# Performance work log

Hardware: AMD Instinct MI355X
Metric: run time of the kernel (lower is better)

The kernel has to match this reference:

```python
import jax, jax.numpy as jnp
import numpy as np

DIM = 256; H = 64; W = 64; NH = 8; NL = 1; NP = 8; HD = DIM // NH
B = 4


def _bilinear(img, grid):
    """torch.grid_sample(mode='bilinear', padding='zeros', align_corners=False).
    img: [C, Hl, Wl]; grid: [N, P, 2] normalized xy in [-1, 1]. Returns [C, N, P]."""
    Hl, Wl = img.shape[1], img.shape[2]
    x = (grid[..., 0] + 1.0) * (Wl * 0.5) - 0.5
    y = (grid[..., 1] + 1.0) * (Hl * 0.5) - 0.5
    x0 = jnp.floor(x); y0 = jnp.floor(y)
    wx = x - x0; wy = y - y0

    def gather(xi, yi):
        valid = (xi >= 0) & (xi < Wl) & (yi >= 0) & (yi < Hl)
        xc = jnp.clip(xi, 0, Wl - 1).astype(jnp.int32)
        yc = jnp.clip(yi, 0, Hl - 1).astype(jnp.int32)
        return img[:, yc, xc] * valid.astype(img.dtype)[None]  # [C, N, P]

    v00 = gather(x0, y0); v01 = gather(x0 + 1, y0)
    v10 = gather(x0, y0 + 1); v11 = gather(x0 + 1, y0 + 1)
    top = v00 * (1.0 - wx) + v01 * wx
    bot = v10 * (1.0 - wx) + v11 * wx
    return top * (1.0 - wy) + bot * wy


def _msda(value, loc, att):
    """multi_scale_deformable_attn_pytorch.
    value: [b, nv, NH, HD]; loc: [b, nq, NH, NL, NP, 2] in [0,1]; att: [b, nq, NH, NL, NP]."""
    b, nv, _, _ = value.shape
    nq = loc.shape[1]
    grids = 2.0 * loc - 1.0
    bn = b * NH
    level_shapes = [(H, W)] * NL  # all levels share the single [H, W] grid here
    sampled_levels = []
    offset = 0
    for l, (Hl, Wl) in enumerate(level_shapes):
        vl = value[:, offset:offset + Hl * Wl]                     # [b, HW, NH, HD]
        offset += Hl * Wl
        vl = vl.transpose(0, 2, 3, 1).reshape(bn, HD, Hl, Wl)      # [b*NH, HD, Hl, Wl]
        gl = grids[:, :, :, l].transpose(0, 2, 1, 3, 4).reshape(bn, nq, NP, 2)
        sampled_levels.append(jax.vmap(_bilinear)(vl, gl))         # [b*NH, HD, nq, NP]
    sampled = jnp.stack(sampled_levels, axis=3)                    # [b*NH, HD, nq, NL, NP]
    w = att.transpose(0, 2, 1, 3, 4).reshape(bn, 1, nq, NL, NP)
    out = jnp.sum(sampled * w, axis=(3, 4))                        # [b*NH, HD, nq]
    return out.reshape(b, NH, HD, nq).transpose(0, 3, 1, 2).reshape(b, nq, NH * HD)


def _forward(query, value, W_loc, b_loc, W_att, b_att, W_val, b_val, W_out, b_out):
    b = query.shape[0]
    nq = H * W
    q = query.transpose(0, 2, 3, 1).reshape(b, nq, DIM)
    v = value.transpose(0, 2, 3, 1).reshape(b, nq, DIM)
    loc = (q @ W_loc.T + b_loc).reshape(b, nq, NH, NL, NP, 2)
    att = jax.nn.softmax((q @ W_att.T + b_att).reshape(b, nq, NH, NL * NP), axis=-1)
    att = att.reshape(b, nq, NH, NL, NP)
    v = (v @ W_val.T + b_val).reshape(b, nq, NH, HD)
    out = _msda(v, loc, att)                                       # [b, nq, DIM]
    return out @ W_out.T + b_out


def setup_inputs() -> dict:
    key = jax.random.key(0)
    ks = jax.random.split(key, 12)
    s = 0.02
    return {
        "query": jax.random.normal(ks[0], (B, DIM, H, W), jnp.float32),
        "value": jax.random.normal(ks[1], (B, DIM, H, W), jnp.float32),
        "W_loc": jax.random.normal(ks[2], (NH * NL * NP * 2, DIM), jnp.float32) * s,
        "b_loc": jax.random.normal(ks[3], (NH * NL * NP * 2,), jnp.float32) * s,
        "W_att": jax.random.normal(ks[4], (NH * NL * NP, DIM), jnp.float32) * s,
        "b_att": jax.random.normal(ks[5], (NH * NL * NP,), jnp.float32) * s,
        "W_val": jax.random.normal(ks[6], (DIM, DIM), jnp.float32) * s,
        "b_val": jax.random.normal(ks[7], (DIM,), jnp.float32) * s,
        "W_out": jax.random.normal(ks[8], (DIM, DIM), jnp.float32) * s,
        "b_out": jax.random.normal(ks[9], (DIM,), jnp.float32) * s,
    }


def reference(query, value, W_loc, b_loc, W_att, b_att, W_val, b_val, W_out, b_out):
    return _forward(query, value, W_loc, b_loc, W_att, b_att, W_val, b_val, W_out, b_out)
```

## Files before the change

### kernel.cpp

```cpp
#include <hip/hip_runtime.h>
#include <hip/hip_bf16.h>
#include <math.h>

#define NQ   4096
#define DIMC 256
#define NHC  8
#define NPC  8
#define HDC  32
#define HC   64
#define WC   64
#define BC   4

typedef __bf16 bf16x8 __attribute__((ext_vector_type(8)));
typedef __attribute__((ext_vector_type(4))) float f4;
typedef __attribute__((ext_vector_type(2))) float v2f;
typedef __attribute__((ext_vector_type(8))) short s8v;

__device__ __forceinline__ ushort f2bf(float f) {
  __hip_bfloat16 h = __float2bfloat16(f);
  union { __hip_bfloat16 h; ushort u; } c; c.h = h; return c.u;
}
__device__ __forceinline__ float bflo(unsigned u) {
  union { unsigned i; float f; } c; c.i = u << 16; return c.f;
}
__device__ __forceinline__ float bfhi(unsigned u) {
  union { unsigned i; float f; } c; c.i = u & 0xffff0000u; return c.f;
}

__global__ __launch_bounds__(256) void k_locatt(
    const float* __restrict__ query,
    const float* __restrict__ W_loc, const float* __restrict__ b_loc,
    const float* __restrict__ W_att, const float* __restrict__ b_att,
    float* __restrict__ loc, float* __restrict__ att) {
  __shared__ float Xs[16][136];
  __shared__ float Ws[16][72];
  const int b  = blockIdx.z;
  const int n0 = blockIdx.x * 128;
  const int o0 = blockIdx.y * 64;
  const int tid = threadIdx.x;
  const int xk = tid >> 4, xn = (tid & 15) * 8;
  const int wo = tid >> 2, wk = (tid & 3) * 4;
  const int tn = (tid & 15) * 8;
  const int to = (tid >> 4) * 4;
  const float* Xb = query + (size_t)b * DIMC * NQ;
  const int oo = o0 + wo;
  const float* Wrow = (oo < 128) ? (W_loc + (size_t)oo * DIMC)
                                 : (W_att + (size_t)(oo - 128) * DIMC);

  v2f acc[8][2];
#pragma unroll
  for (int i = 0; i < 8; ++i) { acc[i][0] = (v2f)0.f; acc[i][1] = (v2f)0.f; }

  for (int k0 = 0; k0 < DIMC; k0 += 16) {
    float4 xv0 = *(const float4*)(Xb + (size_t)(k0 + xk) * NQ + n0 + xn);
    float4 xv1 = *(const float4*)(Xb + (size_t)(k0 + xk) * NQ + n0 + xn + 4);
    float4 wv  = *(const float4*)(Wrow + k0 + wk);
    __syncthreads();
    *(float4*)(&Xs[xk][xn])     = xv0;
    *(float4*)(&Xs[xk][xn + 4]) = xv1;
    Ws[wk + 0][wo] = wv.x; Ws[wk + 1][wo] = wv.y;
    Ws[wk + 2][wo] = wv.z; Ws[wk + 3][wo] = wv.w;
    __syncthreads();
#pragma unroll
    for (int k = 0; k < 16; ++k) {
      float4 xa = *(const float4*)(&Xs[k][tn]);
      float4 xb = *(const float4*)(&Xs[k][tn + 4]);
      v2f w01 = *(const v2f*)(&Ws[k][to]);
      v2f w23 = *(const v2f*)(&Ws[k][to + 2]);
      float xr[8] = {xa.x, xa.y, xa.z, xa.w, xb.x, xb.y, xb.z, xb.w};
#pragma unroll
      for (int i = 0; i < 8; ++i) {
        v2f xi = {xr[i], xr[i]};
        acc[i][0] = xi * w01 + acc[i][0];
        acc[i][1] = xi * w23 + acc[i][1];
      }
    }
  }
  const int obase = o0 + to;
  if (obase < 128) {
    float4 bias = *(const float4*)(b_loc + obase);
#pragma unroll
    for (int i = 0; i < 8; ++i) {
      const int n = n0 + tn + i;
      float4 r = {acc[i][0].x + bias.x, acc[i][0].y + bias.y,
                  acc[i][1].x + bias.z, acc[i][1].y + bias.w};
      *(float4*)(loc + ((size_t)b * NQ + n) * 128 + obase) = r;
    }
  } else {
    float4 bias = *(const float4*)(b_att + obase - 128);
#pragma unroll
    for (int i = 0; i < 8; ++i) {
      const int n = n0 + tn + i;
      float4 r = {acc[i][0].x + bias.x, acc[i][0].y + bias.y,
                  acc[i][1].x + bias.z, acc[i][1].y + bias.w};
      *(float4*)(att + ((size_t)b * NQ + n) * 64 + obase - 128) = r;
    }
  }
}

#define LSTR 40
__global__ __launch_bounds__(256) void k_vproj(
    const float* __restrict__ value, const float* __restrict__ W_val,
    const float* __restrict__ b_val, ushort* __restrict__ vproj) {
  __shared__ __align__(16) ushort As[128 * LSTR];
  __shared__ __align__(16) ushort Ws[64 * LSTR];
  const int b  = blockIdx.z;
  const int n0 = blockIdx.x * 128;
  const int o0 = blockIdx.y * 64;
  const int tid = threadIdx.x;
  const int lane = tid & 63, wid = tid >> 6;
  const int wn0 = (wid & 1) * 64, wo0 = (wid >> 1) * 32;
  const int an = tid & 31;
  const int ak = (tid >> 5) * 4;
  const int wo = tid >> 2, wk = (tid & 3) * 8;
  const float* Xb = value + (size_t)b * DIMC * NQ;
  const int am = lane & 15, kq = (lane >> 4) * 8;

  f4 acc[4][2];
#pragma unroll
  for (int mi = 0; mi < 4; ++mi) { acc[mi][0] = (f4)0.f; acc[mi][1] = (f4)0.f; }

  for (int k0 = 0; k0 < DIMC; k0 += 32) {
    float av[4][4];
#pragma unroll
    for (int kk = 0; kk < 4; ++kk)
#pragma unroll
      for (int nn = 0; nn < 4; ++nn)
        av[kk][nn] = Xb[(size_t)(k0 + ak + kk) * NQ + n0 + an + nn * 32];
    float4 w0 = *(const float4*)(W_val + (size_t)(o0 + wo) * DIMC + k0 + wk);
    float4 w1 = *(const float4*)(W_val + (size_t)(o0 + wo) * DIMC + k0 + wk + 4);
    __syncthreads();
#pragma unroll
    for (int nn = 0; nn < 4; ++nn) {
      ushort4 pk;
      pk.x = f2bf(av[0][nn]); pk.y = f2bf(av[1][nn]);
      pk.z = f2bf(av[2][nn]); pk.w = f2bf(av[3][nn]);
      *(ushort4*)(&As[(an + nn * 32) * LSTR + ak]) = pk;
    }
    {
      ushort4 pa, pb;
      pa.x = f2bf(w0.x); pa.y = f2bf(w0.y); pa.z = f2bf(w0.z); pa.w = f2bf(w0.w);
      pb.x = f2bf(w1.x); pb.y = f2bf(w1.y); pb.z = f2bf(w1.z); pb.w = f2bf(w1.w);
      *(ushort4*)(&Ws[wo * LSTR + wk])     = pa;
      *(ushort4*)(&Ws[wo * LSTR + wk + 4]) = pb;
    }
    __syncthreads();
    bf16x8 afr[4], bfr[2];
#pragma unroll
    for (int mi = 0; mi < 4; ++mi)
      afr[mi] = *(const bf16x8*)(&As[(wn0 + mi * 16 + am) * LSTR + kq]);
#pragma unroll
    for (int oj = 0; oj < 2; ++oj)
      bfr[oj] = *(const bf16x8*)(&Ws[(wo0 + oj * 16 + am) * LSTR + kq]);
#pragma unroll
    for (int mi = 0; mi < 4; ++mi)
#pragma unroll
      for (int oj = 0; oj < 2; ++oj)
        acc[mi][oj] = __builtin_amdgcn_mfma_f32_16x16x32_bf16(
            afr[mi], bfr[oj], acc[mi][oj], 0, 0, 0);
  }
#pragma unroll
  for (int oj = 0; oj < 2; ++oj) {
    const int o = o0 + wo0 + oj * 16 + (lane & 15);
    const int h = o >> 5, d = o & 31;
    const float bias = b_val[o];
    ushort* dst = vproj + ((size_t)(b * NHC + h) * NQ) * HDC + d;
#pragma unroll
    for (int mi = 0; mi < 4; ++mi) {
      const int nb = n0 + wn0 + mi * 16 + (lane >> 4) * 4;
#pragma unroll
      for (int r = 0; r < 4; ++r)
        dst[(size_t)(nb + r) * HDC] = f2bf(acc[mi][oj][r] + bias);
    }
  }
}

__global__ __launch_bounds__(256) void k_sample(
    const float* __restrict__ loc, const float* __restrict__ attL,
    const ushort* __restrict__ vproj, ushort* __restrict__ msda) {
  __shared__ float4 Lc[32][9];
  __shared__ int4   Lo[32][9];
  const int b = blockIdx.z, h = blockIdx.y;
  const int tid = threadIdx.x;
  const int n0 = blockIdx.x * 32;
  {
    const int q = tid >> 3, p = tid & 7;
    const int n = n0 + q;
    const float lg = attL[((size_t)b * NQ + n) * 64 + h * 8 + p];
    float m = lg;
#pragma unroll
    for (int off = 1; off < 8; off <<= 1) m = fmaxf(m, __shfl_xor(m, off, 64));
    const float e = __expf(lg - m);
    float s = e;
#pragma unroll
    for (int off = 1; off < 8; off <<= 1) s += __shfl_xor(s, off, 64);
    const float w = e / s;
    const float2 xy = *(const float2*)(loc + ((size_t)b * NQ + n) * 128 + h * 16 + p * 2);
    const float x = xy.x * 64.0f - 0.5f;
    const float y = xy.y * 64.0f - 0.5f;
    const float x0f = floorf(x), y0f = floorf(y);
    const float wx = x - x0f, wy = y - y0f;
    const int x0 = (int)x0f, y0 = (int)y0f;
    const int x1 = x0 + 1, y1 = y0 + 1;
    const float fx0 = (x0 >= 0 && x0 < WC) ? 1.f : 0.f;
    const float fx1 = (x1 >= 0 && x1 < WC) ? 1.f : 0.f;
    const float fy0 = (y0 >= 0 && y0 < HC) ? 1.f : 0.f;
    const float fy1 = (y1 >= 0 && y1 < HC) ? 1.f : 0.f;
    const int cx0 = min(max(x0, 0), WC - 1), cx1 = min(max(x1, 0), WC - 1);
    const int cy0 = min(max(y0, 0), HC - 1), cy1 = min(max(y1, 0), HC - 1);
    float4 cf;
    cf.x = w * (1.f - wx) * (1.f - wy) * fx0 * fy0;
    cf.y = w * wx * (1.f - wy) * fx1 * fy0;
    cf.z = w * (1.f - wx) * wy * fx0 * fy1;
    cf.w = w * wx * wy * fx1 * fy1;
    int4 of;
    of.x = (cy0 * WC + cx0) * HDC; of.y = (cy0 * WC + cx1) * HDC;
    of.z = (cy1 * WC + cx0) * HDC; of.w = (cy1 * WC + cx1) * HDC;
    Lc[q][p] = cf; Lo[q][p] = of;
  }
  __syncthreads();
  const int q = tid >> 3, d4 = (tid & 7) * 4;
  const int n = n0 + q;
  const ushort* vb = vproj + (size_t)((b * NHC + h) * NQ) * HDC + d4;
  float a0 = 0.f, a1 = 0.f, a2 = 0.f, a3 = 0.f;
#pragma unroll
  for (int p = 0; p < 8; ++p) {
    const int4 of = Lo[q][p];
    const float4 cf = Lc[q][p];
    uint2 u00 = *(const uint2*)(vb + of.x);
    uint2 u01 = *(const uint2*)(vb + of.y);
    uint2 u10 = *(const uint2*)(vb + of.z);
    uint2 u11 = *(const uint2*)(vb + of.w);
    a0 += cf.x * bflo(u00.x) + cf.y * bflo(u01.x) + cf.z * bflo(u10.x) + cf.w * bflo(u11.x);
    a1 += cf.x * bfhi(u00.x) + cf.y * bfhi(u01.x) + cf.z * bfhi(u10.x) + cf.w * bfhi(u11.x);
    a2 += cf.x * bflo(u00.y) + cf.y * bflo(u01.y) + cf.z * bflo(u10.y) + cf.w * bflo(u11.y);
    a3 += cf.x * bfhi(u00.y) + cf.y * bfhi(u01.y) + cf.z * bfhi(u10.y) + cf.w * bfhi(u11.y);
  }
  ushort4 r;
  r.x = f2bf(a0); r.y = f2bf(a1); r.z = f2bf(a2); r.w = f2bf(a3);
  *(ushort4*)(msda + ((size_t)b * NQ + n) * DIMC + h * HDC + d4) = r;
}

__global__ __launch_bounds__(256) void k_out(
    const ushort* __restrict__ msda, const float* __restrict__ W_out,
    const float* __restrict__ b_out, float* __restrict__ out) {
  __shared__ __align__(16) ushort As[128 * LSTR];
  __shared__ __align__(16) ushort Ws[64 * LSTR];
  const int b  = blockIdx.z;
  const int n0 = blockIdx.x * 128;
  const int o0 = blockIdx.y * 64;
  const int tid = threadIdx.x;
  const int lane = tid & 63, wid = tid >> 6;
  const int wn0 = (wid & 1) * 64, wo0 = (wid >> 1) * 32;
  const int ar = tid >> 1, akh = (tid & 1) * 16;
  const int wo = tid >> 2, wk = (tid & 3) * 8;
  const int am = lane & 15, kq = (lane >> 4) * 8;
  const ushort* Ab = msda + (size_t)b * NQ * DIMC;

  f4 acc[4][2];
#pragma unroll
  for (int mi = 0; mi < 4; ++mi) { acc[mi][0] = (f4)0.f; acc[mi][1] = (f4)0.f; }

  for (int k0 = 0; k0 < DIMC; k0 += 32) {
    s8v a0 = *(const s8v*)(Ab + (size_t)(n0 + ar) * DIMC + k0 + akh);
    s8v a1 = *(const s8v*)(Ab + (size_t)(n0 + ar) * DIMC + k0 + akh + 8);
    float4 w0 = *(const float4*)(W_out + (size_t)(o0 + wo) * DIMC + k0 + wk);
    float4 w1 = *(const float4*)(W_out + (size_t)(o0 + wo) * DIMC + k0 + wk + 4);
    __syncthreads();
    *(s8v*)(&As[ar * LSTR + akh])     = a0;
    *(s8v*)(&As[ar * LSTR + akh + 8]) = a1;
    {
      ushort4 pa, pb;
      pa.x = f2bf(w0.x); pa.y = f2bf(w0.y); pa.z = f2bf(w0.z); pa.w = f2bf(w0.w);
      pb.x = f2bf(w1.x); pb.y = f2bf(w1.y); pb.z = f2bf(w1.z); pb.w = f2bf(w1.w);
      *(ushort4*)(&Ws[wo * LSTR + wk])     = pa;
      *(ushort4*)(&Ws[wo * LSTR + wk + 4]) = pb;
    }
    __syncthreads();
    bf16x8 afr[4], bfr[2];
#pragma unroll
    for (int mi = 0; mi < 4; ++mi)
      afr[mi] = *(const bf16x8*)(&As[(wn0 + mi * 16 + am) * LSTR + kq]);
#pragma unroll
    for (int oj = 0; oj < 2; ++oj)
      bfr[oj] = *(const bf16x8*)(&Ws[(wo0 + oj * 16 + am) * LSTR + kq]);
#pragma unroll
    for (int mi = 0; mi < 4; ++mi)
#pragma unroll
      for (int oj = 0; oj < 2; ++oj)
        acc[mi][oj] = __builtin_amdgcn_mfma_f32_16x16x32_bf16(
            afr[mi], bfr[oj], acc[mi][oj], 0, 0, 0);
  }
#pragma unroll
  for (int oj = 0; oj < 2; ++oj) {
    const int o = o0 + wo0 + oj * 16 + (lane & 15);
    const float bias = b_out[o];
#pragma unroll
    for (int mi = 0; mi < 4; ++mi) {
      const int nb = n0 + wn0 + mi * 16 + (lane >> 4) * 4;
#pragma unroll
      for (int r = 0; r < 4; ++r)
        out[((size_t)b * NQ + nb + r) * DIMC + o] = acc[mi][oj][r] + bias;
    }
  }
}

extern "C" void kernel_launch(void* const* d_in, const int* in_sizes, int n_in,
                              void* d_out, int out_size, void* d_ws, size_t ws_size,
                              hipStream_t stream) {
  const float* query = (const float*)d_in[0];
  const float* value = (const float*)d_in[1];
  const float* W_loc = (const float*)d_in[2];
  const float* b_loc = (const float*)d_in[3];
  const float* W_att = (const float*)d_in[4];
  const float* b_att = (const float*)d_in[5];
  const float* W_val = (const float*)d_in[6];
  const float* b_val = (const float*)d_in[7];
  const float* W_out = (const float*)d_in[8];
  const float* b_out = (const float*)d_in[9];
  float* out = (float*)d_out;

  float* ws = (float*)d_ws;
  float* loc   = ws;
  float* att   = loc + (size_t)BC * NQ * 128;
  ushort* vproj = (ushort*)(att + (size_t)BC * NQ * 64);
  ushort* msda  = vproj + (size_t)BC * NHC * NQ * HDC;

  dim3 blk(256);
  k_locatt<<<dim3(NQ / 128, 3, BC), blk, 0, stream>>>(query, W_loc, b_loc, W_att, b_att, loc, att);
  k_vproj <<<dim3(NQ / 128, 4, BC), blk, 0, stream>>>(value, W_val, b_val, vproj);
  k_sample<<<dim3(NQ / 32, NHC, BC), blk, 0, stream>>>(loc, att, vproj, msda);
  k_out   <<<dim3(NQ / 128, 4, BC), blk, 0, stream>>>(msda, W_out, b_out, out);
}
```

Baseline: 156.7 us.

## Use split-bf16 MFMA for loc/att GEMM, prefetch tiles, shrink GEMM tiles, widen sampling

The FP32 FMA loc/att projection becomes an MFMA GEMM that splits each operand into high and low bf16 parts and uses three MFMAs per tile to keep near-fp32 accuracy on sampling locations. All three GEMMs move to 64x64 tiles with register prefetch of the next k-slice, overlapping global loads with compute and doubling the block count. The sampling kernel handles 64 queries per block, and each thread gathers 8 bf16 channels with 16-byte loads. The split-precision path costs three MFMAs and extra LDS traffic, and smaller tiles reduce per-block reuse.

```diff
diff --git a/kernel.cpp b/kernel.cpp
--- a/kernel.cpp
+++ b/kernel.cpp
@@ -10,15 +10,18 @@
 #define HC   64
 #define WC   64
 #define BC   4
+#define LSTR 40
 
 typedef __bf16 bf16x8 __attribute__((ext_vector_type(8)));
 typedef __attribute__((ext_vector_type(4))) float f4;
-typedef __attribute__((ext_vector_type(2))) float v2f;
 typedef __attribute__((ext_vector_type(8))) short s8v;
 
 __device__ __forceinline__ ushort f2bf(float f) {
   __hip_bfloat16 h = __float2bfloat16(f);
   union { __hip_bfloat16 h; ushort u; } c; c.h = h; return c.u;
+}
+__device__ __forceinline__ float bfu2f(ushort u) {
+  union { unsigned i; float f; } c; c.i = ((unsigned)u) << 16; return c.f;
 }
 __device__ __forceinline__ float bflo(unsigned u) {
   union { unsigned i; float f; } c; c.i = u << 16; return c.f;
@@ -32,141 +35,167 @@
     const float* __restrict__ W_loc, const float* __restrict__ b_loc,
     const float* __restrict__ W_att, const float* __restrict__ b_att,
     float* __restrict__ loc, float* __restrict__ att) {
-  __shared__ float Xs[16][136];
-  __shared__ float Ws[16][72];
-  const int b  = blockIdx.z;
-  const int n0 = blockIdx.x * 128;
-  const int o0 = blockIdx.y * 64;
-  const int tid = threadIdx.x;
-  const int xk = tid >> 4, xn = (tid & 15) * 8;
-  const int wo = tid >> 2, wk = (tid & 3) * 4;
-  const int tn = (tid & 15) * 8;
-  const int to = (tid >> 4) * 4;
-  const float* Xb = query + (size_t)b * DIMC * NQ;
+  __shared__ __align__(16) ushort Ah[64 * LSTR], Al[64 * LSTR];
+  __shared__ __align__(16) ushort Wh[64 * LSTR], Wl[64 * LSTR];
+  const int b = blockIdx.z, n0 = blockIdx.x * 64, o0 = blockIdx.y * 64;
+  const int tid = threadIdx.x, lane = tid & 63, wid = tid >> 6;
+  const int wn0 = (wid & 1) * 32, wo0 = (wid >> 1) * 32;
+  const int am = lane & 15, kq = (lane >> 4) * 8;
+  const int an = tid & 63, ak = (tid >> 6) * 8;
+  const int wo = tid >> 2, wk = (tid & 3) * 8;
+  const float* Xb = query + (size_t)b * DIMC * NQ + n0 + an;
   const int oo = o0 + wo;
   const float* Wrow = (oo < 128) ? (W_loc + (size_t)oo * DIMC)
                                  : (W_att + (size_t)(oo - 128) * DIMC);
 
-  v2f acc[8][2];
-#pragma unroll
-  for (int i = 0; i < 8; ++i) { acc[i][0] = (v2f)0.f; acc[i][1] = (v2f)0.f; }
-
-  for (int k0 = 0; k0 < DIMC; k0 += 16) {
-    float4 xv0 = *(const float4*)(Xb + (size_t)(k0 + xk) * NQ + n0 + xn);
-    float4 xv1 = *(const float4*)(Xb + (size_t)(k0 + xk) * NQ + n0 + xn + 4);
-    float4 wv  = *(const float4*)(Wrow + k0 + wk);
-    __syncthreads();
-    *(float4*)(&Xs[xk][xn])     = xv0;
-    *(float4*)(&Xs[xk][xn + 4]) = xv1;
-    Ws[wk + 0][wo] = wv.x; Ws[wk + 1][wo] = wv.y;
-    Ws[wk + 2][wo] = wv.z; Ws[wk + 3][wo] = wv.w;
-    __syncthreads();
-#pragma unroll
-    for (int k = 0; k < 16; ++k) {
-      float4 xa = *(const float4*)(&Xs[k][tn]);
-      float4 xb = *(const float4*)(&Xs[k][tn + 4]);
-      v2f w01 = *(const v2f*)(&Ws[k][to]);
-      v2f w23 = *(const v2f*)(&Ws[k][to + 2]);
-      float xr[8] = {xa.x, xa.y, xa.z, xa.w, xb.x, xb.y, xb.z, xb.w};
-#pragma unroll
-      for (int i = 0; i < 8; ++i) {
-        v2f xi = {xr[i], xr[i]};
-        acc[i][0] = xi * w01 + acc[i][0];
-        acc[i][1] = xi * w23 + acc[i][1];
+  f4 acc[2][2];
+#pragma unroll
+  for (int mi = 0; mi < 2; ++mi) { acc[mi][0] = (f4)0.f; acc[mi][1] = (f4)0.f; }
+
+  float ax[8];
+  float4 wx0, wx1;
+#pragma unroll
+  for (int j = 0; j < 8; ++j) ax[j] = Xb[(size_t)(ak + j) * NQ];
+  wx0 = *(const float4*)(Wrow + wk);
+  wx1 = *(const float4*)(Wrow + wk + 4);
+
+  for (int t = 0; t < 8; ++t) {
+    __syncthreads();
+    {
+      union { ushort u[8]; s8v s; } ph, pl;
+#pragma unroll
+      for (int j = 0; j < 8; ++j) {
+        ushort h = f2bf(ax[j]);
+        ph.u[j] = h;
+        pl.u[j] = f2bf(ax[j] - bfu2f(h));
       }
-    }
-  }
-  const int obase = o0 + to;
-  if (obase < 128) {
-    float4 bias = *(const float4*)(b_loc + obase);
-#pragma unroll
-    for (int i = 0; i < 8; ++i) {
-      const int n = n0 + tn + i;
-      float4 r = {acc[i][0].x + bias.x, acc[i][0].y + bias.y,
-                  acc[i][1].x + bias.z, acc[i][1].y + bias.w};
-      *(float4*)(loc + ((size_t)b * NQ + n) * 128 + obase) = r;
-    }
-  } else {
-    float4 bias = *(const float4*)(b_att + obase - 128);
-#pragma unroll
-    for (int i = 0; i < 8; ++i) {
-      const int n = n0 + tn + i;
-      float4 r = {acc[i][0].x + bias.x, acc[i][0].y + bias.y,
-                  acc[i][1].x + bias.z, acc[i][1].y + bias.w};
-      *(float4*)(att + ((size_t)b * NQ + n) * 64 + obase - 128) = r;
-    }
-  }
-}
-
-#define LSTR 40
+      *(s8v*)(&Ah[an * LSTR + ak]) = ph.s;
+      *(s8v*)(&Al[an * LSTR + ak]) = pl.s;
+      float wt[8] = {wx0.x, wx0.y, wx0.z, wx0.w, wx1.x, wx1.y, wx1.z, wx1.w};
+      union { ushort u[8]; s8v s; } qh, ql;
+#pragma unroll
+      for (int j = 0; j < 8; ++j) {
+        ushort h = f2bf(wt[j]);
+        qh.u[j] = h;
+        ql.u[j] = f2bf(wt[j] - bfu2f(h));
+      }
+      *(s8v*)(&Wh[wo * LSTR + wk]) = qh.s;
+      *(s8v*)(&Wl[wo * LSTR + wk]) = ql.s;
+    }
+    if (t < 7) {
+      const int k0 = (t + 1) * 32;
+#pragma unroll
+      for (int j = 0; j < 8; ++j) ax[j] = Xb[(size_t)(k0 + ak + j) * NQ];
+      wx0 = *(const float4*)(Wrow + k0 + wk);
+      wx1 = *(const float4*)(Wrow + k0 + wk + 4);
+    }
+    __syncthreads();
+    bf16x8 ah[2], al[2], bh[2], bl[2];
+#pragma unroll
+    for (int mi = 0; mi < 2; ++mi) {
+      ah[mi] = *(const bf16x8*)(&Ah[(wn0 + mi * 16 + am) * LSTR + kq]);
+      al[mi] = *(const bf16x8*)(&Al[(wn0 + mi * 16 + am) * LSTR + kq]);
+    }
+#pragma unroll
+    for (int oj = 0; oj < 2; ++oj) {
+      bh[oj] = *(const bf16x8*)(&Wh[(wo0 + oj * 16 + am) * LSTR + kq]);
+      bl[oj] = *(const bf16x8*)(&Wl[(wo0 + oj * 16 + am) * LSTR + kq]);
+    }
+#pragma unroll
+    for (int mi = 0; mi < 2; ++mi)
+#pragma unroll
+      for (int oj = 0; oj < 2; ++oj) {
+        acc[mi][oj] = __builtin_amdgcn_mfma_f32_16x16x32_bf16(ah[mi], bh[oj], acc[mi][oj], 0, 0, 0);
+        acc[mi][oj] = __builtin_amdgcn_mfma_f32_16x16x32_bf16(al[mi], bh[oj], acc[mi][oj], 0, 0, 0);
+        acc[mi][oj] = __builtin_amdgcn_mfma_f32_16x16x32_bf16(ah[mi], bl[oj], acc[mi][oj], 0, 0, 0);
+      }
+  }
+  const bool isAtt = (o0 >= 128);
+  float* dstBase = isAtt ? att : loc;
+  const float* bias = isAtt ? b_att : b_loc;
+  const int ostride = isAtt ? 64 : 128;
+  const int ob = isAtt ? o0 - 128 : o0;
+#pragma unroll
+  for (int oj = 0; oj < 2; ++oj) {
+    const int o = ob + wo0 + oj * 16 + am;
+    const float bv = bias[o];
+#pragma unroll
+    for (int mi = 0; mi < 2; ++mi) {
+      const int nb = n0 + wn0 + mi * 16 + (lane >> 4) * 4;
+#pragma unroll
+      for (int r = 0; r < 4; ++r)
+        dstBase[((size_t)b * NQ + nb + r) * ostride + o] = acc[mi][oj][r] + bv;
+    }
+  }
+}
+
 __global__ __launch_bounds__(256) void k_vproj(
     const float* __restrict__ value, const float* __restrict__ W_val,
     const float* __restrict__ b_val, ushort* __restrict__ vproj) {
-  __shared__ __align__(16) ushort As[128 * LSTR];
+  __shared__ __align__(16) ushort As[64 * LSTR];
   __shared__ __align__(16) ushort Ws[64 * LSTR];
-  const int b  = blockIdx.z;
-  const int n0 = blockIdx.x * 128;
-  const int o0 = blockIdx.y * 64;
-  const int tid = threadIdx.x;
-  const int lane = tid & 63, wid = tid >> 6;
-  const int wn0 = (wid & 1) * 64, wo0 = (wid >> 1) * 32;
-  const int an = tid & 31;
-  const int ak = (tid >> 5) * 4;
+  const int b = blockIdx.z, n0 = blockIdx.x * 64, o0 = blockIdx.y * 64;
+  const int tid = threadIdx.x, lane = tid & 63, wid = tid >> 6;
+  const int wn0 = (wid & 1) * 32, wo0 = (wid >> 1) * 32;
+  const int am = lane & 15, kq = (lane >> 4) * 8;
+  const int an = tid & 63, ak = (tid >> 6) * 8;
   const int wo = tid >> 2, wk = (tid & 3) * 8;
-  const float* Xb = value + (size_t)b * DIMC * NQ;
-  const int am = lane & 15, kq = (lane >> 4) * 8;
-
-  f4 acc[4][2];
-#pragma unroll
-  for (int mi = 0; mi < 4; ++mi) { acc[mi][0] = (f4)0.f; acc[mi][1] = (f4)0.f; }
-
-  for (int k0 = 0; k0 < DIMC; k0 += 32) {
-    float av[4][4];
-#pragma unroll
-    for (int kk = 0; kk < 4; ++kk)
-#pragma unroll
-      for (int nn = 0; nn < 4; ++nn)
-        av[kk][nn] = Xb[(size_t)(k0 + ak + kk) * NQ + n0 + an + nn * 32];
-    float4 w0 = *(const float4*)(W_val + (size_t)(o0 + wo) * DIMC + k0 + wk);
-    float4 w1 = *(const float4*)(W_val + (size_t)(o0 + wo) * DIMC + k0 + wk + 4);
-    __syncthreads();
-#pragma unroll
-    for (int nn = 0; nn < 4; ++nn) {
-      ushort4 pk;
-      pk.x = f2bf(av[0][nn]); pk.y = f2bf(av[1][nn]);
-      pk.z = f2bf(av[2][nn]); pk.w = f2bf(av[3][nn]);
-      *(ushort4*)(&As[(an + nn * 32) * LSTR + ak]) = pk;
-    }
+  const float* Xb = value + (size_t)b * DIMC * NQ + n0 + an;
+  const float* Wrow = W_val + (size_t)(o0 + wo) * DIMC;
+
+  f4 acc[2][2];
+#pragma unroll
+  for (int mi = 0; mi < 2; ++mi) { acc[mi][0] = (f4)0.f; acc[mi][1] = (f4)0.f; }
+
+  float ax[8];
+  float4 wx0, wx1;
+#pragma unroll
+  for (int j = 0; j < 8; ++j) ax[j] = Xb[(size_t)(ak + j) * NQ];
+  wx0 = *(const float4*)(Wrow + wk);
+  wx1 = *(const float4*)(Wrow + wk + 4);
+
+  for (int t = 0; t < 8; ++t) {
+    __syncthreads();
     {
-      ushort4 pa, pb;
-      pa.x = f2bf(w0.x); pa.y = f2bf(w0.y); pa.z = f2bf(w0.z); pa.w = f2bf(w0.w);
-      pb.x = f2bf(w1.x); pb.y = f2bf(w1.y); pb.z = f2bf(w1.z); pb.w = f2bf(w1.w);
-      *(ushort4*)(&Ws[wo * LSTR + wk])     = pa;
-      *(ushort4*)(&Ws[wo * LSTR + wk + 4]) = pb;
-    }
-    __syncthreads();
-    bf16x8 afr[4], bfr[2];
-#pragma unroll
-    for (int mi = 0; mi < 4; ++mi)
-      afr[mi] = *(const bf16x8*)(&As[(wn0 + mi * 16 + am) * LSTR + kq]);
+      union { ushort u[8]; s8v s; } pa;
+#pragma unroll
+      for (int j = 0; j < 8; ++j) pa.u[j] = f2bf(ax[j]);
+      *(s8v*)(&As[an * LSTR + ak]) = pa.s;
+      float wt[8] = {wx0.x, wx0.y, wx0.z, wx0.w, wx1.x, wx1.y, wx1.z, wx1.w};
+      union { ushort u[8]; s8v s; } pw;
+#pragma unroll
+      for (int j = 0; j < 8; ++j) pw.u[j] = f2bf(wt[j]);
+      *(s8v*)(&Ws[wo * LSTR + wk]) = pw.s;
+    }
+    if (t < 7) {
+      const int k0 = (t + 1) * 32;
+#pragma unroll
+      for (int j = 0; j < 8; ++j) ax[j] = Xb[(size_t)(k0 + ak + j) * NQ];
+      wx0 = *(const float4*)(Wrow + k0 + wk);
+      wx1 = *(const float4*)(Wrow + k0 + wk + 4);
+    }
+    __syncthreads();
+    bf16x8 af[2], bf[2];
+#pragma unroll
+    for (int mi = 0; mi < 2; ++mi)
+      af[mi] = *(const bf16x8*)(&As[(wn0 + mi * 16 + am) * LSTR + kq]);
 #pragma unroll
     for (int oj = 0; oj < 2; ++oj)
-      bfr[oj] = *(const bf16x8*)(&Ws[(wo0 + oj * 16 + am) * LSTR + kq]);
-#pragma unroll
-    for (int mi = 0; mi < 4; ++mi)
+      bf[oj] = *(const bf16x8*)(&Ws[(wo0 + oj * 16 + am) * LSTR + kq]);
+#pragma unroll
+    for (int mi = 0; mi < 2; ++mi)
 #pragma unroll
       for (int oj = 0; oj < 2; ++oj)
-        acc[mi][oj] = __builtin_amdgcn_mfma_f32_16x16x32_bf16(
-            afr[mi], bfr[oj], acc[mi][oj], 0, 0, 0);
+        acc[mi][oj] = __builtin_amdgcn_mfma_f32_16x16x32_bf16(af[mi], bf[oj], acc[mi][oj], 0, 0, 0);
   }
 #pragma unroll
   for (int oj = 0; oj < 2; ++oj) {
-    const int o = o0 + wo0 + oj * 16 + (lane & 15);
+    const int o = o0 + wo0 + oj * 16 + am;
     const int h = o >> 5, d = o & 31;
     const float bias = b_val[o];
     ushort* dst = vproj + ((size_t)(b * NHC + h) * NQ) * HDC + d;
 #pragma unroll
-    for (int mi = 0; mi < 4; ++mi) {
+    for (int mi = 0; mi < 2; ++mi) {
       const int nb = n0 + wn0 + mi * 16 + (lane >> 4) * 4;
 #pragma unroll
       for (int r = 0; r < 4; ++r)
@@ -178,13 +207,15 @@
 __global__ __launch_bounds__(256) void k_sample(
     const float* __restrict__ loc, const float* __restrict__ attL,
     const ushort* __restrict__ vproj, ushort* __restrict__ msda) {
-  __shared__ float4 Lc[32][9];
-  __shared__ int4   Lo[32][9];
+  __shared__ float4 Lc[64][9];
+  __shared__ int4   Lo[64][9];
   const int b = blockIdx.z, h = blockIdx.y;
   const int tid = threadIdx.x;
-  const int n0 = blockIdx.x * 32;
-  {
-    const int q = tid >> 3, p = tid & 7;
+  const int n0 = blockIdx.x * 64;
+#pragma unroll
+  for (int it = 0; it < 2; ++it) {
+    const int idx = it * 256 + tid;
+    const int q = idx >> 3, p = idx & 7;
     const int n = n0 + q;
     const float lg = attL[((size_t)b * NQ + n) * 64 + h * 8 + p];
     float m = lg;
@@ -219,84 +250,92 @@
     Lc[q][p] = cf; Lo[q][p] = of;
   }
   __syncthreads();
-  const int q = tid >> 3, d4 = (tid & 7) * 4;
+  const int q = tid >> 2, d8 = (tid & 3) * 8;
   const int n = n0 + q;
-  const ushort* vb = vproj + (size_t)((b * NHC + h) * NQ) * HDC + d4;
-  float a0 = 0.f, a1 = 0.f, a2 = 0.f, a3 = 0.f;
+  const ushort* vb = vproj + (size_t)((b * NHC + h) * NQ) * HDC + d8;
+  float a[8] = {};
 #pragma unroll
   for (int p = 0; p < 8; ++p) {
     const int4 of = Lo[q][p];
     const float4 cf = Lc[q][p];
-    uint2 u00 = *(const uint2*)(vb + of.x);
-    uint2 u01 = *(const uint2*)(vb + of.y);
-    uint2 u10 = *(const uint2*)(vb + of.z);
-    uint2 u11 = *(const uint2*)(vb + of.w);
-    a0 += cf.x * bflo(u00.x) + cf.y * bflo(u01.x) + cf.z * bflo(u10.x) + cf.w * bflo(u11.x);
-    a1 += cf.x * bfhi(u00.x) + cf.y * bfhi(u01.x) + cf.z * bfhi(u10.x) + cf.w * bfhi(u11.x);
-    a2 += cf.x * bflo(u00.y) + cf.y * bflo(u01.y) + cf.z * bflo(u10.y) + cf.w * bflo(u11.y);
-    a3 += cf.x * bfhi(u00.y) + cf.y * bfhi(u01.y) + cf.z * bfhi(u10.y) + cf.w * bfhi(u11.y);
-  }
-  ushort4 r;
-  r.x = f2bf(a0); r.y = f2bf(a1); r.z = f2bf(a2); r.w = f2bf(a3);
-  *(ushort4*)(msda + ((size_t)b * NQ + n) * DIMC + h * HDC + d4) = r;
+    const uint4 u00 = *(const uint4*)(vb + of.x);
+    const uint4 u01 = *(const uint4*)(vb + of.y);
+    const uint4 u10 = *(const uint4*)(vb + of.z);
+    const uint4 u11 = *(const uint4*)(vb + of.w);
+    const unsigned c00[4] = {u00.x, u00.y, u00.z, u00.w};
+    const unsigned c01[4] = {u01.x, u01.y, u01.z, u01.w};
+    const unsigned c10[4] = {u10.x, u10.y, u10.z, u10.w};
+    const unsigned c11[4] = {u11.x, u11.y, u11.z, u11.w};
+#pragma unroll
+    for (int j = 0; j < 4; ++j) {
+      a[2 * j]     += cf.x * bflo(c00[j]) + cf.y * bflo(c01[j]) + cf.z * bflo(c10[j]) + cf.w * bflo(c11[j]);
+      a[2 * j + 1] += cf.x * bfhi(c00[j]) + cf.y * bfhi(c01[j]) + cf.z * bfhi(c10[j]) + cf.w * bfhi(c11[j]);
+    }
+  }
+  union { ushort u[8]; s8v s; } r;
+#pragma unroll
+  for (int j = 0; j < 8; ++j) r.u[j] = f2bf(a[j]);
+  *(s8v*)(msda + ((size_t)b * NQ + n) * DIMC + h * HDC + d8) = r.s;
 }
 
 __global__ __launch_bounds__(256) void k_out(
     const ushort* __restrict__ msda, const float* __restrict__ W_out,
     const float* __restrict__ b_out, float* __restrict__ out) {
-  __shared__ __align__(16) ushort As[128 * LSTR];
+  __shared__ __align__(16) ushort As[64 * LSTR];
   __shared__ __align__(16) ushort Ws[64 * LSTR];
-  const int b  = blockIdx.z;
-  const int n0 = blockIdx.x * 128;
-  const int o0 = blockIdx.y * 64;
-  const int tid = threadIdx.x;
-  const int lane = tid & 63, wid = tid >> 6;
-  const int wn0 = (wid & 1) * 64, wo0 = (wid >> 1) * 32;
-  const int ar = tid >> 1, akh = (tid & 1) * 16;
+  const int b = blockIdx.z, n0 = blockIdx.x * 64, o0 = blockIdx.y * 64;
+  const int tid = threadIdx.x, lane = tid & 63, wid = tid >> 6;
+  const int wn0 = (wid & 1) * 32, wo0 = (wid >> 1) * 32;
+  const int am = lane & 15, kq = (lane >> 4) * 8;
+  const int ar = tid >> 2, akq = (tid & 3) * 8;
   const int wo = tid >> 2, wk = (tid & 3) * 8;
-  const int am = lane & 15, kq = (lane >> 4) * 8;
-  const ushort* Ab = msda + (size_t)b * NQ * DIMC;
-
-  f4 acc[4][2];
-#pragma unroll
-  for (int mi = 0; mi < 4; ++mi) { acc[mi][0] = (f4)0.f; acc[mi][1] = (f4)0.f; }
-
-  for (int k0 = 0; k0 < DIMC; k0 += 32) {
-    s8v a0 = *(const s8v*)(Ab + (size_t)(n0 + ar) * DIMC + k0 + akh);
-    s8v a1 = *(const s8v*)(Ab + (size_t)(n0 + ar) * DIMC + k0 + akh + 8);
-    float4 w0 = *(const float4*)(W_out + (size_t)(o0 + wo) * DIMC + k0 + wk);
-    float4 w1 = *(const float4*)(W_out + (size_t)(o0 + wo) * DIMC + k0 + wk + 4);
-    __syncthreads();
-    *(s8v*)(&As[ar * LSTR + akh])     = a0;
-    *(s8v*)(&As[ar * LSTR + akh + 8]) = a1;
+  const ushort* Ab = msda + ((size_t)b * NQ + n0 + ar) * DIMC + akq;
+  const float* Wrow = W_out + (size_t)(o0 + wo) * DIMC;
+
+  f4 acc[2][2];
+#pragma unroll
+  for (int mi = 0; mi < 2; ++mi) { acc[mi][0] = (f4)0.f; acc[mi][1] = (f4)0.f; }
+
+  s8v aval = *(const s8v*)(Ab);
+  float4 wx0 = *(const float4*)(Wrow + wk);
+  float4 wx1 = *(const float4*)(Wrow + wk + 4);
+
+  for (int t = 0; t < 8; ++t) {
+    __syncthreads();
+    *(s8v*)(&As[ar * LSTR + akq]) = aval;
     {
-      ushort4 pa, pb;
-      pa.x = f2bf(w0.x); pa.y = f2bf(w0.y); pa.z = f2bf(w0.z); pa.w = f2bf(w0.w);
-      pb.x = f2bf(w1.x); pb.y = f2bf(w1.y); pb.z = f2bf(w1.z); pb.w = f2bf(w1.w);
-      *(ushort4*)(&Ws[wo * LSTR + wk])     = pa;
-      *(ushort4*)(&Ws[wo * LSTR + wk + 4]) = pb;
-    }
-    __syncthreads();
-    bf16x8 afr[4], bfr[2];
-#pragma unroll
-    for (int mi = 0; mi < 4; ++mi)
-      afr[mi] = *(const bf16x8*)(&As[(wn0 + mi * 16 + am) * LSTR + kq]);
+      float wt[8] = {wx0.x, wx0.y, wx0.z, wx0.w, wx1.x, wx1.y, wx1.z, wx1.w};
+      union { ushort u[8]; s8v s; } pw;
+#pragma unroll
+      for (int j = 0; j < 8; ++j) pw.u[j] = f2bf(wt[j]);
+      *(s8v*)(&Ws[wo * LSTR + wk]) = pw.s;
+    }
+    if (t < 7) {
+      const int k0 = (t + 1) * 32;
+      aval = *(const s8v*)(Ab + k0);
+      wx0 = *(const float4*)(Wrow + k0 + wk);
+      wx1 = *(const float4*)(Wrow + k0 + wk + 4);
+    }
+    __syncthreads();
+    bf16x8 af[2], bf[2];
+#pragma unroll
+    for (int mi = 0; mi < 2; ++mi)
+      af[mi] = *(const bf16x8*)(&As[(wn0 + mi * 16 + am) * LSTR + kq]);
 #pragma unroll
     for (int oj = 0; oj < 2; ++oj)
-      bfr[oj] = *(const bf16x8*)(&Ws[(wo0 + oj * 16 + am) * LSTR + kq]);
-#pragma unroll
-    for (int mi = 0; mi < 4; ++mi)
+      bf[oj] = *(const bf16x8*)(&Ws[(wo0 + oj * 16 + am) * LSTR + kq]);
+#pragma unroll
+    for (int mi = 0; mi < 2; ++mi)
 #pragma unroll
       for (int oj = 0; oj < 2; ++oj)
-        acc[mi][oj] = __builtin_amdgcn_mfma_f32_16x16x32_bf16(
-            afr[mi], bfr[oj], acc[mi][oj], 0, 0, 0);
+        acc[mi][oj] = __builtin_amdgcn_mfma_f32_16x16x32_bf16(af[mi], bf[oj], acc[mi][oj], 0, 0, 0);
   }
 #pragma unroll
   for (int oj = 0; oj < 2; ++oj) {
-    const int o = o0 + wo0 + oj * 16 + (lane & 15);
+    const int o = o0 + wo0 + oj * 16 + am;
     const float bias = b_out[o];
 #pragma unroll
-    for (int mi = 0; mi < 4; ++mi) {
+    for (int mi = 0; mi < 2; ++mi) {
       const int nb = n0 + wn0 + mi * 16 + (lane >> 4) * 4;
 #pragma unroll
       for (int r = 0; r < 4; ++r)
@@ -321,14 +360,14 @@
   float* out = (float*)d_out;
 
   float* ws = (float*)d_ws;
-  float* loc   = ws;
-  float* att   = loc + (size_t)BC * NQ * 128;
+  float* loc    = ws;
+  float* att    = loc + (size_t)BC * NQ * 128;
   ushort* vproj = (ushort*)(att + (size_t)BC * NQ * 64);
   ushort* msda  = vproj + (size_t)BC * NHC * NQ * HDC;
 
   dim3 blk(256);
-  k_locatt<<<dim3(NQ / 128, 3, BC), blk, 0, stream>>>(query, W_loc, b_loc, W_att, b_att, loc, att);
-  k_vproj <<<dim3(NQ / 128, 4, BC), blk, 0, stream>>>(value, W_val, b_val, vproj);
-  k_sample<<<dim3(NQ / 32, NHC, BC), blk, 0, stream>>>(loc, att, vproj, msda);
-  k_out   <<<dim3(NQ / 128, 4, BC), blk, 0, stream>>>(msda, W_out, b_out, out);
-}
+  k_locatt<<<dim3(NQ / 64, 3, BC), blk, 0, stream>>>(query, W_loc, b_loc, W_att, b_att, loc, att);
+  k_vproj <<<dim3(NQ / 64, 4, BC), blk, 0, stream>>>(value, W_val, b_val, vproj);
+  k_sample<<<dim3(NQ / 64, NHC, BC), blk, 0, stream>>>(loc, att, vproj, msda);
+  k_out   <<<dim3(NQ / 64, 4, BC), blk, 0, stream>>>(msda, W_out, b_out, out);
+}
```

New measurement: 130.7 us. 16.6% less time.
